# Kernel optimization log

Measured on AMD Instinct MI355X. Metric: run time of the kernel, lower is better.

## Reference

```python
import jax, jax.numpy as jnp
import numpy as np

N_NODES = 50000
N_EDGES = 400000
N_GRAPHS = 500
N_FEAT = 4
EMB = 200
HID = 128


def setup_inputs() -> dict:
    key = jax.random.key(0)
    ks = jax.random.split(key, 16)
    x = jax.random.normal(ks[0], (N_NODES, N_FEAT), dtype=jnp.float32)
    edge_index = jax.random.randint(ks[1], (2, N_EDGES), 0, N_NODES, dtype=jnp.int64)
    x_scalar = jax.random.normal(ks[2], (N_GRAPHS, N_FEAT), dtype=jnp.float32)
    batch_index = jnp.sort(jax.random.randint(ks[3], (N_NODES,), 0, N_GRAPHS, dtype=jnp.int64))

    def lin(k, fan_in, fan_out):
        return jax.random.normal(k, (fan_in, fan_out), dtype=jnp.float32) / np.sqrt(fan_in)

    params = {
        'W0': lin(ks[4], N_FEAT, EMB), 'b0': jnp.zeros((EMB,), jnp.float32),
        'W1': lin(ks[5], EMB, EMB), 'b1': jnp.zeros((EMB,), jnp.float32),
        'W2': lin(ks[6], EMB, EMB), 'b2': jnp.zeros((EMB,), jnp.float32),
        'W3': lin(ks[7], EMB, EMB), 'b3': jnp.zeros((EMB,), jnp.float32),
        'Wl1': lin(ks[8], EMB + N_FEAT, HID),
        'bl1': jax.random.normal(ks[9], (HID,), jnp.float32) * 0.01,
        'Wl2': lin(ks[10], HID, 1),
        'bl2': jax.random.normal(ks[11], (1,), jnp.float32) * 0.01,
    }
    return dict(x=x, edge_index=edge_index, x_scalar=x_scalar, batch_index=batch_index, **params)


def _gcn_conv(h, W, b, src, dst, norm, num_nodes):
    # PyG GCNConv: h' = D^-1/2 (A+I) D^-1/2 (h W) + b, with precomputed edge norms
    m = (h @ W)[src] * norm[:, None]            # [E+N, out]
    out = jax.ops.segment_sum(m, dst, num_segments=num_nodes)
    return out + b


def reference(x, edge_index, x_scalar, batch_index,
              W0, b0, W1, b1, W2, b2, W3, b3, Wl1, bl1, Wl2, bl2):
    num_nodes = x.shape[0]
    loops = jnp.arange(num_nodes, dtype=edge_index.dtype)
    src = jnp.concatenate([edge_index[0], loops])  # self-loops appended
    dst = jnp.concatenate([edge_index[1], loops])
    deg = jax.ops.segment_sum(jnp.ones_like(dst, dtype=x.dtype), dst, num_segments=num_nodes)
    dinv = deg ** -0.5                              # deg >= 1 due to self-loops
    norm = dinv[src] * dinv[dst]

    h = jax.nn.leaky_relu(_gcn_conv(x, W0, b0, src, dst, norm, num_nodes), 0.01)
    h = jax.nn.leaky_relu(_gcn_conv(h, W1, b1, src, dst, norm, num_nodes), 0.01)
    h = jax.nn.leaky_relu(_gcn_conv(h, W2, b2, src, dst, norm, num_nodes), 0.01)
    h = jax.nn.leaky_relu(_gcn_conv(h, W3, b3, src, dst, norm, num_nodes), 0.01)

    # global mean pool per graph
    sums = jax.ops.segment_sum(h, batch_index, num_segments=N_GRAPHS)
    cnt = jax.ops.segment_sum(jnp.ones((num_nodes,), h.dtype), batch_index, num_segments=N_GRAPHS)
    pooled = sums / jnp.maximum(cnt, 1.0)[:, None]

    g = jnp.concatenate([pooled, x_scalar], axis=1)   # [G, EMB+4]
    g = jax.nn.leaky_relu(g @ Wl1 + bl1, 0.01)
    out = g @ Wl2 + bl2                                # [G, 1]
    return out
```

## Files before the change

kernel.cpp:

```cpp
#include <hip/hip_runtime.h>
#include <math.h>

#define LEAKY(v) ((v) > 0.0f ? (v) : 0.01f * (v))

typedef _Float16 v8h __attribute__((ext_vector_type(8)));
typedef float v4f __attribute__((ext_vector_type(4)));

__global__ void k_count(const int* __restrict__ ei, int* __restrict__ cnt, int E) {
    int e = blockIdx.x * blockDim.x + threadIdx.x;
    if (e < E) atomicAdd(&cnt[ei[E + e]], 1);
}

__global__ __launch_bounds__(256) void k_scan1(const int* __restrict__ cnt,
                                               int* __restrict__ rowptr,
                                               int* __restrict__ bsum, int n) {
    __shared__ int s[256];
    int t = threadIdx.x, i = blockIdx.x * 256 + t;
    int v = (i < n) ? cnt[i] : 0;
    s[t] = v;
    __syncthreads();
    for (int off = 1; off < 256; off <<= 1) {
        int u = (t >= off) ? s[t - off] : 0;
        __syncthreads();
        s[t] += u;
        __syncthreads();
    }
    if (i < n) rowptr[i] = s[t] - v;
    if (t == 255) bsum[blockIdx.x] = s[255];
}

__global__ __launch_bounds__(256) void k_scan2(int* __restrict__ bsum, int nb) {
    __shared__ int s[256];
    int t = threadIdx.x;
    int v = (t < nb) ? bsum[t] : 0;
    s[t] = v;
    __syncthreads();
    for (int off = 1; off < 256; off <<= 1) {
        int u = (t >= off) ? s[t - off] : 0;
        __syncthreads();
        s[t] += u;
        __syncthreads();
    }
    if (t < nb) bsum[t] = s[t] - v;
}

__global__ __launch_bounds__(256) void k_scan3(int* __restrict__ rowptr,
                                               const int* __restrict__ bsum,
                                               const int* __restrict__ cnt,
                                               float* __restrict__ dinv, int n) {
    int i = blockIdx.x * 256 + threadIdx.x;
    if (i < n) {
        rowptr[i] += bsum[blockIdx.x];
        dinv[i] = rsqrtf(1.0f + (float)cnt[i]);
    }
}

__global__ void k_fill(const int* __restrict__ ei, const float* __restrict__ dinv,
                       int* __restrict__ rowptr, int2* __restrict__ adj, int E) {
    int e = blockIdx.x * blockDim.x + threadIdx.x;
    if (e < E) {
        int s = ei[e], d = ei[E + e];
        int pos = atomicAdd(&rowptr[d], 1);
        adj[pos] = make_int2(s, __float_as_int(dinv[s] * dinv[d]));
    }
}

__global__ __launch_bounds__(256) void k_splitW3(const float* __restrict__ W1,
                                                 const float* __restrict__ W2,
                                                 const float* __restrict__ W3,
                                                 _Float16* __restrict__ th0, _Float16* __restrict__ tl0,
                                                 _Float16* __restrict__ th1, _Float16* __restrict__ tl1,
                                                 _Float16* __restrict__ th2, _Float16* __restrict__ tl2,
                                                 int* __restrict__ cnt, int n) {
    int layer = blockIdx.y;
    const float* W = (layer == 0) ? W1 : (layer == 1) ? W2 : W3;
    _Float16* Wth = (layer == 0) ? th0 : (layer == 1) ? th1 : th2;
    _Float16* Wtl = (layer == 0) ? tl0 : (layer == 1) ? tl1 : tl2;
    int idx = blockIdx.x * blockDim.x + threadIdx.x;
    int gidx = (blockIdx.y * gridDim.x + blockIdx.x) * 256 + threadIdx.x;
    for (int j = gidx; j < n; j += gridDim.x * gridDim.y * 256) cnt[j] = 0;
    if (idx >= 224 * 208) return;
    int k = idx / 208, c = idx - k * 208;
    float v = (k < 200 && c < 200) ? W[k * 200 + c] : 0.0f;
    _Float16 hi = (_Float16)v;
    _Float16 lo = (_Float16)(v - (float)hi);
    Wth[c * 224 + k] = hi;
    Wtl[c * 224 + k] = lo;
}

__global__ __launch_bounds__(512, 2) void k_gemm200_mfma_l0(const float* __restrict__ x,
                                                            const float* __restrict__ dinv,
                                                            const int* __restrict__ rowptr,
                                                            const int2* __restrict__ adj,
                                                            const float* __restrict__ W0,
                                                            const float* __restrict__ b0,
                                                            const _Float16* __restrict__ Wth,
                                                            const _Float16* __restrict__ Wtl,
                                                            _Float16* __restrict__ T, int M) {
    __shared__ _Float16 Wsh[208 * 32];
    __shared__ _Float16 Wsl[208 * 32];
    __shared__ float W0s[4][200];
    __shared__ float b0s[200];
    const int tid  = threadIdx.x;
    const int lane = tid & 63;
    const int wid  = tid >> 6;
    const int quad = lane >> 4;
    const int l16  = lane & 15;
    const int rowA = blockIdx.x * 128 + wid * 16 + l16;
    const int rowAc = min(rowA, M - 1);

    float w0n = dinv[rowAc]; w0n *= w0n;
    float4 xv = ((const float4*)x)[rowAc];
    float4 pxv = make_float4(xv.x * w0n, xv.y * w0n, xv.z * w0n, xv.w * w0n);
    {
        int lo = rowAc ? rowptr[rowAc - 1] : 0;
        int hi = rowptr[rowAc];
        for (int j = lo; j < hi; ++j) {
            int2 cw = adj[j];
            float w = __int_as_float(cw.y);
            float4 sv = ((const float4*)x)[cw.x];
            pxv.x += sv.x * w; pxv.y += sv.y * w; pxv.z += sv.z * w; pxv.w += sv.w * w;
        }
    }

    for (int idx = tid; idx < 1000; idx += 512) {
        if (idx < 800) W0s[idx / 200][idx % 200] = W0[idx];
        else b0s[idx - 800] = b0[idx - 800];
    }
    __syncthreads();

    v4f acc[13];
#pragma unroll
    for (int t = 0; t < 13; ++t) acc[t] = 0.0f;

    for (int k0 = 0; k0 < 224; k0 += 32) {
        v8h ah, al;
        int kb = k0 + quad * 8;
        if (kb < 200) {
#pragma unroll
            for (int j = 0; j < 8; ++j) {
                int k = kb + j;
                float pv = pxv.x * W0s[0][k] + pxv.y * W0s[1][k]
                         + pxv.z * W0s[2][k] + pxv.w * W0s[3][k] + b0s[k];
                pv = LEAKY(pv);
                _Float16 h = (_Float16)pv;
                ah[j] = h;
                al[j] = (_Float16)(pv - (float)h);
            }
        } else {
#pragma unroll
            for (int j = 0; j < 8; ++j) { ah[j] = (_Float16)0.0f; al[j] = (_Float16)0.0f; }
        }
        __syncthreads();
        for (int idx = tid; idx < 832; idx += 512) {
            int nr = idx >> 2, part = idx & 3;
            *(uint4*)&Wsh[nr * 32 + part * 8] = *(const uint4*)&Wth[nr * 224 + k0 + part * 8];
            *(uint4*)&Wsl[nr * 32 + part * 8] = *(const uint4*)&Wtl[nr * 224 + k0 + part * 8];
        }
        __syncthreads();
#pragma unroll
        for (int t = 0; t < 13; ++t) {
            int nidx = (t * 16 + l16) * 32 + quad * 8;
            v8h wh = *(const v8h*)&Wsh[nidx];
            v8h wl = *(const v8h*)&Wsl[nidx];
            acc[t] = __builtin_amdgcn_mfma_f32_16x16x32_f16(ah, wh, acc[t], 0, 0, 0);
            acc[t] = __builtin_amdgcn_mfma_f32_16x16x32_f16(ah, wl, acc[t], 0, 0, 0);
            acc[t] = __builtin_amdgcn_mfma_f32_16x16x32_f16(al, wh, acc[t], 0, 0, 0);
        }
    }
    const int rb = blockIdx.x * 128 + wid * 16 + quad * 4;
#pragma unroll
    for (int t = 0; t < 13; ++t) {
        int c = t * 16 + l16;
        if (c < 200) {
#pragma unroll
            for (int e = 0; e < 4; ++e) {
                int r = rb + e;
                if (r < M) T[(size_t)r * 200 + c] = (_Float16)acc[t][e];
            }
        }
    }
}

__global__ __launch_bounds__(512, 2) void k_gemm200_mfma(const _Float16* __restrict__ P,
                                                         const float* __restrict__ bias,
                                                         const _Float16* __restrict__ Wth,
                                                         const _Float16* __restrict__ Wtl,
                                                         _Float16* __restrict__ T, int M) {
    __shared__ _Float16 Wsh[208 * 32];
    __shared__ _Float16 Wsl[208 * 32];
    const int tid  = threadIdx.x;
    const int lane = tid & 63;
    const int wid  = tid >> 6;
    const int quad = lane >> 4;
    const int l16  = lane & 15;
    const int rowA = blockIdx.x * 128 + wid * 16 + l16;
    const int rowAc = min(rowA, M - 1);
    const _Float16* Prow = P + (size_t)rowAc * 200;

    v4f acc[13];
#pragma unroll
    for (int t = 0; t < 13; ++t) acc[t] = 0.0f;

    for (int k0 = 0; k0 < 224; k0 += 32) {
        v8h ah, al;
        int kb = k0 + quad * 8;
        if (kb < 200) {
            v8h ph = *(const v8h*)(Prow + kb);
            float4 ba = *(const float4*)(bias + kb);
            float4 bb = *(const float4*)(bias + kb + 4);
            float bv[8] = {ba.x, ba.y, ba.z, ba.w, bb.x, bb.y, bb.z, bb.w};
#pragma unroll
            for (int j = 0; j < 8; ++j) {
                float av = (float)ph[j] + bv[j];
                av = LEAKY(av);
                _Float16 h = (_Float16)av;
                ah[j] = h;
                al[j] = (_Float16)(av - (float)h);
            }
        } else {
#pragma unroll
            for (int j = 0; j < 8; ++j) { ah[j] = (_Float16)0.0f; al[j] = (_Float16)0.0f; }
        }
        __syncthreads();
        for (int idx = tid; idx < 832; idx += 512) {
            int nr = idx >> 2, part = idx & 3;
            *(uint4*)&Wsh[nr * 32 + part * 8] = *(const uint4*)&Wth[nr * 224 + k0 + part * 8];
            *(uint4*)&Wsl[nr * 32 + part * 8] = *(const uint4*)&Wtl[nr * 224 + k0 + part * 8];
        }
        __syncthreads();
#pragma unroll
        for (int t = 0; t < 13; ++t) {
            int nidx = (t * 16 + l16) * 32 + quad * 8;
            v8h wh = *(const v8h*)&Wsh[nidx];
            v8h wl = *(const v8h*)&Wsl[nidx];
            acc[t] = __builtin_amdgcn_mfma_f32_16x16x32_f16(ah, wh, acc[t], 0, 0, 0);
            acc[t] = __builtin_amdgcn_mfma_f32_16x16x32_f16(ah, wl, acc[t], 0, 0, 0);
            acc[t] = __builtin_amdgcn_mfma_f32_16x16x32_f16(al, wh, acc[t], 0, 0, 0);
        }
    }
    const int rb = blockIdx.x * 128 + wid * 16 + quad * 4;
#pragma unroll
    for (int t = 0; t < 13; ++t) {
        int c = t * 16 + l16;
        if (c < 200) {
#pragma unroll
            for (int e = 0; e < 4; ++e) {
                int r = rb + e;
                if (r < M) T[(size_t)r * 200 + c] = (_Float16)acc[t][e];
            }
        }
    }
}

__global__ __launch_bounds__(256) void k_gather200h(const _Float16* __restrict__ t,
                                                    const float* __restrict__ dinv,
                                                    const int* __restrict__ rowptr,
                                                    const int2* __restrict__ adj,
                                                    _Float16* __restrict__ p, int n) {
    int gid = blockIdx.x * blockDim.x + threadIdx.x;
    if (gid >= n * 25) return;
    int v = gid / 25, c8 = gid - v * 25;
    const v8h* tp = (const v8h*)t;
    float w0 = dinv[v]; w0 *= w0;
    v8h tv = tp[v * 25 + c8];
    float a0[8], a1[8], a2[8], a3[8];
#pragma unroll
    for (int i = 0; i < 8; ++i) { a0[i] = (float)tv[i] * w0; a1[i] = 0.0f; a2[i] = 0.0f; a3[i] = 0.0f; }
    int lo = v ? rowptr[v - 1] : 0;
    int hi = rowptr[v];
    int j = lo;
    for (; j + 3 < hi; j += 4) {
        int2 e0 = adj[j], e1 = adj[j + 1], e2 = adj[j + 2], e3 = adj[j + 3];
        float wa = __int_as_float(e0.y), wb = __int_as_float(e1.y);
        float wc = __int_as_float(e2.y), wd = __int_as_float(e3.y);
        v8h s0 = tp[e0.x * 25 + c8];
        v8h s1 = tp[e1.x * 25 + c8];
        v8h s2 = tp[e2.x * 25 + c8];
        v8h s3 = tp[e3.x * 25 + c8];
#pragma unroll
        for (int i = 0; i < 8; ++i) {
            a0[i] += (float)s0[i] * wa;
            a1[i] += (float)s1[i] * wb;
            a2[i] += (float)s2[i] * wc;
            a3[i] += (float)s3[i] * wd;
        }
    }
    for (; j < hi; ++j) {
        int2 cw = adj[j];
        float w = __int_as_float(cw.y);
        v8h sv = tp[cw.x * 25 + c8];
#pragma unroll
        for (int i = 0; i < 8; ++i) a0[i] += (float)sv[i] * w;
    }
    v8h o;
#pragma unroll
    for (int i = 0; i < 8; ++i) o[i] = (_Float16)((a0[i] + a1[i]) + (a2[i] + a3[i]));
    ((v8h*)p)[v * 25 + c8] = o;
}

__global__ __launch_bounds__(256) void k_poolhead(const _Float16* __restrict__ T,
                                                  const float* __restrict__ b3,
                                                  const int* __restrict__ batch, int n,
                                                  const float* __restrict__ xs,
                                                  const float* __restrict__ Wl1,
                                                  const float* __restrict__ bl1,
                                                  const float* __restrict__ Wl2,
                                                  const float* __restrict__ bl2,
                                                  float* __restrict__ out) {
    __shared__ float part[10][25][9];
    __shared__ float grow[204];
    __shared__ float partial[2];
    __shared__ int sb[2];
    int g = blockIdx.x;
    int t = threadIdx.x;
    if (t == 0 || t == 64) {
        int target = g + (t ? 1 : 0);
        int lo = 0, hi = n;
        while (lo < hi) { int m = (lo + hi) >> 1; if (batch[m] < target) lo = m + 1; else hi = m; }
        sb[t ? 1 : 0] = lo;
    }
    __syncthreads();
    int lo = sb[0], hi = sb[1];
    int c8 = t % 25, li = t / 25;
    if (li < 10) {
        const v8h* tp = (const v8h*)T;
        float4 ba = *(const float4*)(b3 + c8 * 8);
        float4 bb = *(const float4*)(b3 + c8 * 8 + 4);
        float bv[8] = {ba.x, ba.y, ba.z, ba.w, bb.x, bb.y, bb.z, bb.w};
        float acc[8];
#pragma unroll
        for (int i = 0; i < 8; ++i) acc[i] = 0.0f;
        for (int i = lo + li; i < hi; i += 10) {
            v8h tv = tp[(size_t)i * 25 + c8];
#pragma unroll
            for (int jj = 0; jj < 8; ++jj) {
                float v = (float)tv[jj] + bv[jj];
                acc[jj] += LEAKY(v);
            }
        }
#pragma unroll
        for (int jj = 0; jj < 8; ++jj) part[li][c8][jj] = acc[jj];
    }
    __syncthreads();
    if (t < 200) {
        float s = 0.0f;
#pragma unroll
        for (int l2 = 0; l2 < 10; ++l2) s += part[l2][t >> 3][t & 7];
        grow[t] = s / fmaxf((float)(hi - lo), 1.0f);
    } else if (t < 204) {
        grow[t] = xs[g * 4 + (t - 200)];
    }
    __syncthreads();
    if (t < 128) {
        float s = bl1[t];
        for (int k = 0; k < 204; ++k) s += grow[k] * Wl1[k * 128 + t];
        s = LEAKY(s);
        float hv = s * Wl2[t];
        for (int off = 32; off > 0; off >>= 1) hv += __shfl_down(hv, off, 64);
        if ((t & 63) == 0) partial[t >> 6] = hv;
    }
    __syncthreads();
    if (t == 0) out[g] = partial[0] + partial[1] + bl2[0];
}

extern "C" void kernel_launch(void* const* d_in, const int* in_sizes, int n_in,
                              void* d_out, int out_size, void* d_ws, size_t ws_size,
                              hipStream_t stream) {
    const float* x    = (const float*)d_in[0];
    const int*   ei   = (const int*)d_in[1];
    const float* xs   = (const float*)d_in[2];
    const int*   batch= (const int*)d_in[3];
    const float* W0   = (const float*)d_in[4];
    const float* b0   = (const float*)d_in[5];
    const float* W1   = (const float*)d_in[6];
    const float* b1   = (const float*)d_in[7];
    const float* W2   = (const float*)d_in[8];
    const float* b2   = (const float*)d_in[9];
    const float* W3   = (const float*)d_in[10];
    const float* b3   = (const float*)d_in[11];
    const float* Wl1  = (const float*)d_in[12];
    const float* bl1  = (const float*)d_in[13];
    const float* Wl2  = (const float*)d_in[14];
    const float* bl2  = (const float*)d_in[15];
    float* out = (float*)d_out;

    const int N = in_sizes[0] / 4;
    const int E = in_sizes[1] / 2;
    const int G = in_sizes[2] / 4;

    char* ws = (char*)d_ws;
    size_t off = 0;
    auto alloc = [&](size_t bytes) { void* p = ws + off; off += (bytes + 255) & ~size_t(255); return p; };
    _Float16* bufA = (_Float16*)alloc((size_t)N * 200 * sizeof(_Float16));
    _Float16* bufB = (_Float16*)alloc((size_t)N * 200 * sizeof(_Float16));
    float* dinv   = (float*)alloc((size_t)N * sizeof(float));
    int*   cnt    = (int*)alloc((size_t)N * sizeof(int));
    int*   rowptr = (int*)alloc(((size_t)N + 1) * sizeof(int));
    int*   bsum   = (int*)alloc(256 * sizeof(int));
    int2*  adj    = (int2*)alloc((size_t)E * sizeof(int2));
    _Float16* Wth[3]; _Float16* Wtl[3];
    for (int i = 0; i < 3; ++i) {
        Wth[i] = (_Float16*)alloc(208 * 224 * sizeof(_Float16));
        Wtl[i] = (_Float16*)alloc(208 * 224 * sizeof(_Float16));
    }

    const int B = 256;
    const int nblk = (N + 255) / 256;

    dim3 sg((224 * 208 + B - 1) / B, 3);
    k_splitW3<<<sg, B, 0, stream>>>(W1, W2, W3, Wth[0], Wtl[0], Wth[1], Wtl[1], Wth[2], Wtl[2],
                                    cnt, N);

    k_count<<<(E + B - 1) / B, B, 0, stream>>>(ei, cnt, E);
    k_scan1<<<nblk, 256, 0, stream>>>(cnt, rowptr, bsum, N);
    k_scan2<<<1, 256, 0, stream>>>(bsum, nblk);
    k_scan3<<<nblk, 256, 0, stream>>>(rowptr, bsum, cnt, dinv, N);
    k_fill<<<(E + B - 1) / B, B, 0, stream>>>(ei, dinv, rowptr, adj, E);

    const int gblocks = (N * 25 + 255) / 256;
    const int mblocks = (N + 127) / 128;

    k_gemm200_mfma_l0<<<mblocks, 512, 0, stream>>>(x, dinv, rowptr, adj, W0, b0,
                                                   Wth[0], Wtl[0], bufA, N);
    k_gather200h<<<gblocks, 256, 0, stream>>>(bufA, dinv, rowptr, adj, bufB, N);

    k_gemm200_mfma<<<mblocks, 512, 0, stream>>>(bufB, b1, Wth[1], Wtl[1], bufA, N);
    k_gather200h<<<gblocks, 256, 0, stream>>>(bufA, dinv, rowptr, adj, bufB, N);
    k_gemm200_mfma<<<mblocks, 512, 0, stream>>>(bufB, b2, Wth[2], Wtl[2], bufA, N);
    k_gather200h<<<gblocks, 256, 0, stream>>>(bufA, dinv, rowptr, adj, bufB, N);

    k_poolhead<<<G, 256, 0, stream>>>(bufB, b3, batch, N, xs, Wl1, bl1, Wl2, bl2, out);
}
```

Baseline: 337.3 us.

## Double-buffer weight tiles in MFMA GEMMs and fold scan2 into scan3

Both MFMA GEMM kernels now double-buffer the weight K-chunks in shared memory and prefetch the next chunk into registers during the current chunk's MFMAs, which cuts one barrier per iteration. The GEMM kernel also preloads all A-row chunks and stages the bias in LDS, and launch bounds go from 2 to 4 blocks per CU. The separate block-sum scan kernel is removed: each scan3 block reduces the preceding block sums itself, which saves a launch. The costs are extra register pressure under the tighter occupancy bound and twice the LDS per block.

```diff
diff --git a/kernel.cpp b/kernel.cpp
--- a/kernel.cpp
+++ b/kernel.cpp
@@ -29,28 +29,24 @@
     if (t == 255) bsum[blockIdx.x] = s[255];
 }
 
-__global__ __launch_bounds__(256) void k_scan2(int* __restrict__ bsum, int nb) {
-    __shared__ int s[256];
-    int t = threadIdx.x;
-    int v = (t < nb) ? bsum[t] : 0;
-    s[t] = v;
-    __syncthreads();
-    for (int off = 1; off < 256; off <<= 1) {
-        int u = (t >= off) ? s[t - off] : 0;
-        __syncthreads();
-        s[t] += u;
-        __syncthreads();
-    }
-    if (t < nb) bsum[t] = s[t] - v;
-}
-
 __global__ __launch_bounds__(256) void k_scan3(int* __restrict__ rowptr,
                                                const int* __restrict__ bsum,
                                                const int* __restrict__ cnt,
                                                float* __restrict__ dinv, int n) {
-    int i = blockIdx.x * 256 + threadIdx.x;
+    __shared__ int sred[256];
+    int t = threadIdx.x;
+    int accum = 0;
+    for (int b = t; b < (int)blockIdx.x; b += 256) accum += bsum[b];
+    sred[t] = accum;
+    __syncthreads();
+    for (int off = 128; off > 0; off >>= 1) {
+        if (t < off) sred[t] += sred[t + off];
+        __syncthreads();
+    }
+    int base = sred[0];
+    int i = blockIdx.x * 256 + t;
     if (i < n) {
-        rowptr[i] += bsum[blockIdx.x];
+        rowptr[i] += base;
         dinv[i] = rsqrtf(1.0f + (float)cnt[i]);
     }
 }
@@ -88,7 +84,7 @@
     Wtl[c * 224 + k] = lo;
 }
 
-__global__ __launch_bounds__(512, 2) void k_gemm200_mfma_l0(const float* __restrict__ x,
+__global__ __launch_bounds__(512, 4) void k_gemm200_mfma_l0(const float* __restrict__ x,
                                                             const float* __restrict__ dinv,
                                                             const int* __restrict__ rowptr,
                                                             const int2* __restrict__ adj,
@@ -97,8 +93,8 @@
                                                             const _Float16* __restrict__ Wth,
                                                             const _Float16* __restrict__ Wtl,
                                                             _Float16* __restrict__ T, int M) {
-    __shared__ _Float16 Wsh[208 * 32];
-    __shared__ _Float16 Wsl[208 * 32];
+    __shared__ _Float16 Wsh[2][208 * 32];
+    __shared__ _Float16 Wsl[2][208 * 32];
     __shared__ float W0s[4][200];
     __shared__ float b0s[200];
     const int tid  = threadIdx.x;
@@ -108,6 +104,22 @@
     const int l16  = lane & 15;
     const int rowA = blockIdx.x * 128 + wid * 16 + l16;
     const int rowAc = min(rowA, M - 1);
+
+    const int nr0 = tid >> 2, p0 = tid & 3;
+    const bool two = (tid < 320);
+    const int nr1 = nr0 + 128;
+    uint4 rh0, rl0, rh1, rl1;
+    rh0 = *(const uint4*)&Wth[nr0 * 224 + p0 * 8];
+    rl0 = *(const uint4*)&Wtl[nr0 * 224 + p0 * 8];
+    if (two) {
+        rh1 = *(const uint4*)&Wth[nr1 * 224 + p0 * 8];
+        rl1 = *(const uint4*)&Wtl[nr1 * 224 + p0 * 8];
+    }
+
+    for (int idx = tid; idx < 1000; idx += 512) {
+        if (idx < 800) W0s[idx / 200][idx % 200] = W0[idx];
+        else b0s[idx - 800] = b0[idx - 800];
+    }
 
     float w0n = dinv[rowAc]; w0n *= w0n;
     float4 xv = ((const float4*)x)[rowAc];
@@ -123,17 +135,29 @@
         }
     }
 
-    for (int idx = tid; idx < 1000; idx += 512) {
-        if (idx < 800) W0s[idx / 200][idx % 200] = W0[idx];
-        else b0s[idx - 800] = b0[idx - 800];
-    }
-    __syncthreads();
-
     v4f acc[13];
 #pragma unroll
     for (int t = 0; t < 13; ++t) acc[t] = 0.0f;
 
-    for (int k0 = 0; k0 < 224; k0 += 32) {
+#pragma unroll
+    for (int kc = 0; kc < 7; ++kc) {
+        const int k0 = kc * 32;
+        const int buf = kc & 1;
+        *(uint4*)&Wsh[buf][nr0 * 32 + p0 * 8] = rh0;
+        *(uint4*)&Wsl[buf][nr0 * 32 + p0 * 8] = rl0;
+        if (two) {
+            *(uint4*)&Wsh[buf][nr1 * 32 + p0 * 8] = rh1;
+            *(uint4*)&Wsl[buf][nr1 * 32 + p0 * 8] = rl1;
+        }
+        if (kc < 6) {
+            rh0 = *(const uint4*)&Wth[nr0 * 224 + (k0 + 32) + p0 * 8];
+            rl0 = *(const uint4*)&Wtl[nr0 * 224 + (k0 + 32) + p0 * 8];
+            if (two) {
+                rh1 = *(const uint4*)&Wth[nr1 * 224 + (k0 + 32) + p0 * 8];
+                rl1 = *(const uint4*)&Wtl[nr1 * 224 + (k0 + 32) + p0 * 8];
+            }
+        }
+        __syncthreads();
         v8h ah, al;
         int kb = k0 + quad * 8;
         if (kb < 200) {
@@ -151,18 +175,11 @@
 #pragma unroll
             for (int j = 0; j < 8; ++j) { ah[j] = (_Float16)0.0f; al[j] = (_Float16)0.0f; }
         }
-        __syncthreads();
-        for (int idx = tid; idx < 832; idx += 512) {
-            int nr = idx >> 2, part = idx & 3;
-            *(uint4*)&Wsh[nr * 32 + part * 8] = *(const uint4*)&Wth[nr * 224 + k0 + part * 8];
-            *(uint4*)&Wsl[nr * 32 + part * 8] = *(const uint4*)&Wtl[nr * 224 + k0 + part * 8];
-        }
-        __syncthreads();
 #pragma unroll
         for (int t = 0; t < 13; ++t) {
             int nidx = (t * 16 + l16) * 32 + quad * 8;
-            v8h wh = *(const v8h*)&Wsh[nidx];
-            v8h wl = *(const v8h*)&Wsl[nidx];
+            v8h wh = *(const v8h*)&Wsh[buf][nidx];
+            v8h wl = *(const v8h*)&Wsl[buf][nidx];
             acc[t] = __builtin_amdgcn_mfma_f32_16x16x32_f16(ah, wh, acc[t], 0, 0, 0);
             acc[t] = __builtin_amdgcn_mfma_f32_16x16x32_f16(ah, wl, acc[t], 0, 0, 0);
             acc[t] = __builtin_amdgcn_mfma_f32_16x16x32_f16(al, wh, acc[t], 0, 0, 0);
@@ -182,13 +199,14 @@
     }
 }
 
-__global__ __launch_bounds__(512, 2) void k_gemm200_mfma(const _Float16* __restrict__ P,
+__global__ __launch_bounds__(512, 4) void k_gemm200_mfma(const _Float16* __restrict__ P,
                                                          const float* __restrict__ bias,
                                                          const _Float16* __restrict__ Wth,
                                                          const _Float16* __restrict__ Wtl,
                                                          _Float16* __restrict__ T, int M) {
-    __shared__ _Float16 Wsh[208 * 32];
-    __shared__ _Float16 Wsl[208 * 32];
+    __shared__ _Float16 Wsh[2][208 * 32];
+    __shared__ _Float16 Wsl[2][208 * 32];
+    __shared__ float bS[200];
     const int tid  = threadIdx.x;
     const int lane = tid & 63;
     const int wid  = tid >> 6;
@@ -198,21 +216,60 @@
     const int rowAc = min(rowA, M - 1);
     const _Float16* Prow = P + (size_t)rowAc * 200;
 
+    const int nr0 = tid >> 2, p0 = tid & 3;
+    const bool two = (tid < 320);
+    const int nr1 = nr0 + 128;
+    uint4 rh0, rl0, rh1, rl1;
+    rh0 = *(const uint4*)&Wth[nr0 * 224 + p0 * 8];
+    rl0 = *(const uint4*)&Wtl[nr0 * 224 + p0 * 8];
+    if (two) {
+        rh1 = *(const uint4*)&Wth[nr1 * 224 + p0 * 8];
+        rl1 = *(const uint4*)&Wtl[nr1 * 224 + p0 * 8];
+    }
+    if (tid < 200) bS[tid] = bias[tid];
+
+    v8h pch[7];
+#pragma unroll
+    for (int kc = 0; kc < 7; ++kc) {
+        int kb = kc * 32 + quad * 8;
+        if (kb < 200) {
+            pch[kc] = *(const v8h*)(Prow + kb);
+        } else {
+#pragma unroll
+            for (int j = 0; j < 8; ++j) pch[kc][j] = (_Float16)0.0f;
+        }
+    }
+
     v4f acc[13];
 #pragma unroll
     for (int t = 0; t < 13; ++t) acc[t] = 0.0f;
 
-    for (int k0 = 0; k0 < 224; k0 += 32) {
+#pragma unroll
+    for (int kc = 0; kc < 7; ++kc) {
+        const int k0 = kc * 32;
+        const int buf = kc & 1;
+        *(uint4*)&Wsh[buf][nr0 * 32 + p0 * 8] = rh0;
+        *(uint4*)&Wsl[buf][nr0 * 32 + p0 * 8] = rl0;
+        if (two) {
+            *(uint4*)&Wsh[buf][nr1 * 32 + p0 * 8] = rh1;
+            *(uint4*)&Wsl[buf][nr1 * 32 + p0 * 8] = rl1;
+        }
+        if (kc < 6) {
+            rh0 = *(const uint4*)&Wth[nr0 * 224 + (k0 + 32) + p0 * 8];
+            rl0 = *(const uint4*)&Wtl[nr0 * 224 + (k0 + 32) + p0 * 8];
+            if (two) {
+                rh1 = *(const uint4*)&Wth[nr1 * 224 + (k0 + 32) + p0 * 8];
+                rl1 = *(const uint4*)&Wtl[nr1 * 224 + (k0 + 32) + p0 * 8];
+            }
+        }
+        __syncthreads();
         v8h ah, al;
         int kb = k0 + quad * 8;
         if (kb < 200) {
-            v8h ph = *(const v8h*)(Prow + kb);
-            float4 ba = *(const float4*)(bias + kb);
-            float4 bb = *(const float4*)(bias + kb + 4);
-            float bv[8] = {ba.x, ba.y, ba.z, ba.w, bb.x, bb.y, bb.z, bb.w};
+            v8h ph = pch[kc];
 #pragma unroll
             for (int j = 0; j < 8; ++j) {
-                float av = (float)ph[j] + bv[j];
+                float av = (float)ph[j] + bS[kb + j];
                 av = LEAKY(av);
                 _Float16 h = (_Float16)av;
                 ah[j] = h;
@@ -222,18 +279,11 @@
 #pragma unroll
             for (int j = 0; j < 8; ++j) { ah[j] = (_Float16)0.0f; al[j] = (_Float16)0.0f; }
         }
-        __syncthreads();
-        for (int idx = tid; idx < 832; idx += 512) {
-            int nr = idx >> 2, part = idx & 3;
-            *(uint4*)&Wsh[nr * 32 + part * 8] = *(const uint4*)&Wth[nr * 224 + k0 + part * 8];
-            *(uint4*)&Wsl[nr * 32 + part * 8] = *(const uint4*)&Wtl[nr * 224 + k0 + part * 8];
-        }
-        __syncthreads();
 #pragma unroll
         for (int t = 0; t < 13; ++t) {
             int nidx = (t * 16 + l16) * 32 + quad * 8;
-            v8h wh = *(const v8h*)&Wsh[nidx];
-            v8h wl = *(const v8h*)&Wsl[nidx];
+            v8h wh = *(const v8h*)&Wsh[buf][nidx];
+            v8h wl = *(const v8h*)&Wsl[buf][nidx];
             acc[t] = __builtin_amdgcn_mfma_f32_16x16x32_f16(ah, wh, acc[t], 0, 0, 0);
             acc[t] = __builtin_amdgcn_mfma_f32_16x16x32_f16(ah, wl, acc[t], 0, 0, 0);
             acc[t] = __builtin_amdgcn_mfma_f32_16x16x32_f16(al, wh, acc[t], 0, 0, 0);
@@ -414,7 +464,6 @@
 
     k_count<<<(E + B - 1) / B, B, 0, stream>>>(ei, cnt, E);
     k_scan1<<<nblk, 256, 0, stream>>>(cnt, rowptr, bsum, N);
-    k_scan2<<<1, 256, 0, stream>>>(bsum, nblk);
     k_scan3<<<nblk, 256, 0, stream>>>(rowptr, bsum, cnt, dinv, N);
     k_fill<<<(E + B - 1) / B, B, 0, stream>>>(ei, dinv, rowptr, adj, E);
 
```

Result: no change. 331.6 us (-1.7%).
